# Kernel tuning notes

Measured on AMD Instinct MI355X. Metric: run time of the kernel, lower is better.

Reference implementation:

```python
import jax, jax.numpy as jnp
from jax import lax
import numpy as np

H = 256

def _cell(x, h, c, wih, whh, bih, bhh):
    # PyTorch LSTMCell: gates ordered i, f, g, o
    g = x @ wih.T + bih + h @ whh.T + bhh
    i, f, gg, o = jnp.split(g, 4, axis=-1)
    c = jax.nn.sigmoid(f) * c + jax.nn.sigmoid(i) * jnp.tanh(gg)
    h = jax.nn.sigmoid(o) * jnp.tanh(c)
    return h, c


def setup_inputs() -> dict:
    key = jax.random.key(0)
    ks = iter(jax.random.split(key, 64))
    def lin(out_f, in_f):
        s = 1.0 / np.sqrt(in_f)
        w = jax.random.uniform(next(ks), (out_f, in_f), minval=-s, maxval=s, dtype=jnp.float32)
        b = jax.random.uniform(next(ks), (out_f,), minval=-s, maxval=s, dtype=jnp.float32)
        return w, b
    def cellp():
        s = 1.0 / np.sqrt(H)
        return tuple(jax.random.uniform(next(ks), sh, minval=-s, maxval=s, dtype=jnp.float32)
                     for sh in [(4 * H, H), (4 * H, H), (4 * H,), (4 * H,)])
    d = {}
    d['x'] = jax.random.normal(next(ks), (20, 256, 64, 64), dtype=jnp.float32)
    d['fc_en1_w'], d['fc_en1_b'] = lin(1024, 4096)
    d['fc_en2_w'], d['fc_en2_b'] = lin(H, 1024)
    for nm in ['en1', 'en2', 'en3', 'de1', 'de2', 'de3']:
        d[nm + '_wih'], d[nm + '_whh'], d[nm + '_bih'], d[nm + '_bhh'] = cellp()
    d['fc_de1_w'], d['fc_de1_b'] = lin(1024, H)
    d['fc_de2_w'], d['fc_de2_b'] = lin(4096, 1024)
    d['future_step'] = 10
    return d


def reference(x, fc_en1_w, fc_en1_b, fc_en2_w, fc_en2_b,
              en1_wih, en1_whh, en1_bih, en1_bhh,
              en2_wih, en2_whh, en2_bih, en2_bhh,
              en3_wih, en3_whh, en3_bih, en3_bhh,
              de1_wih, de1_whh, de1_bih, de1_bhh,
              de2_wih, de2_whh, de2_bih, de2_bhh,
              de3_wih, de3_whh, de3_bih, de3_bhh,
              fc_de1_w, fc_de1_b, fc_de2_w, fc_de2_b, future_step):
    seq, B = x.shape[0], x.shape[1]
    xf = x.reshape(seq, B, -1)  # (S, B, 4096)
    z0 = jnp.zeros((B, H), x.dtype)

    def enc_step(carry, xt):
        h1, c1, h2, c2, h3, c3 = carry
        z = jax.nn.relu(xt @ fc_en1_w.T + fc_en1_b)
        z = jax.nn.relu(z @ fc_en2_w.T + fc_en2_b)
        h1, c1 = _cell(z, h1, c1, en1_wih, en1_whh, en1_bih, en1_bhh)
        h2, c2 = _cell(h1, h2, c2, en2_wih, en2_whh, en2_bih, en2_bhh)
        h3, c3 = _cell(h2, h3, c3, en3_wih, en3_whh, en3_bih, en3_bhh)
        return (h1, c1, h2, c2, h3, c3), None

    enc_carry, _ = lax.scan(enc_step, (z0,) * 6, xf)
    h_e3 = enc_carry[4]

    def dec_step(carry, _):
        h1, c1, h2, c2, h3, c3 = carry
        h1, c1 = _cell(z0, h1, c1, de1_wih, de1_whh, de1_bih, de1_bhh)
        h2, c2 = _cell(h1, h2, c2, de2_wih, de2_whh, de2_bih, de2_bhh)
        h3, c3 = _cell(h2, h3, c3, de3_wih, de3_whh, de3_bih, de3_bhh)
        y = jax.nn.relu(h3 @ fc_de1_w.T + fc_de1_b)
        y = jnp.tanh(y @ fc_de2_w.T + fc_de2_b)
        return (h1, c1, h2, c2, h3, c3), y

    _, ys = lax.scan(dec_step, (h_e3, z0, z0, z0, z0, z0), None, length=future_step)
    return ys.reshape(future_step, B, 64, 64)
```

## Files before the change

### kernel.cpp

```cpp
#include <hip/hip_runtime.h>
#include <math.h>

static __device__ __forceinline__ float sigf(float v) { return 1.0f / (1.0f + expf(-v)); }

using s8v = __attribute__((ext_vector_type(8))) short;
using f4v = __attribute__((ext_vector_type(4))) float;

static __device__ __forceinline__ void splitf(float f, unsigned short& h, unsigned short& l) {
  unsigned u = __float_as_uint(f);
  unsigned short hb = (unsigned short)((u + 0x7FFFu + ((u >> 16) & 1u)) >> 16);
  float hf = __uint_as_float(((unsigned)hb) << 16);
  float lf = f - hf;
  unsigned ul = __float_as_uint(lf);
  unsigned short lb = (unsigned short)((ul + 0x7FFFu + ((ul >> 16) & 1u)) >> 16);
  h = hb; l = lb;
}

__global__ __launch_bounds__(256) void wsplit(
    const float* __restrict__ W, unsigned short* __restrict__ WH,
    unsigned short* __restrict__ WL, int n4)
{
  int i = blockIdx.x * 256 + threadIdx.x;
  if (i < n4) {
    float4 v = ((const float4*)W)[i];
    ushort4 h, l;
    splitf(v.x, h.x, l.x); splitf(v.y, h.y, l.y);
    splitf(v.z, h.z, l.z); splitf(v.w, h.w, l.w);
    ((ushort4*)WH)[i] = h;
    ((ushort4*)WL)[i] = l;
  }
}

template <int OSPLIT>
__global__ __launch_bounds__(256) void gemm_sf(
    const float* __restrict__ A,
    const unsigned short* __restrict__ WH, const unsigned short* __restrict__ WL,
    const float* __restrict__ bias, float* __restrict__ C,
    unsigned short* __restrict__ OH, unsigned short* __restrict__ OL,
    int M, int N, int K, int act)
{
  __shared__ unsigned short AsH[128 * 40];
  __shared__ unsigned short AsL[128 * 40];
  __shared__ unsigned short WsH[64 * 40];
  __shared__ unsigned short WsL[64 * 40];

  const int t = threadIdx.x;
  const int w = t >> 6, lane = t & 63;
  const int lrow = lane & 15, lk = (lane >> 4) * 8;
  const int m0 = blockIdx.x * 128, n0 = blockIdx.y * 64;

  f4v acc[2][4];
#pragma unroll
  for (int i = 0; i < 2; ++i)
#pragma unroll
    for (int j = 0; j < 4; ++j) acc[i][j] = (f4v){0.f, 0.f, 0.f, 0.f};

  for (int k0 = 0; k0 < K; k0 += 32) {
#pragma unroll
    for (int i = 0; i < 4; ++i) {
      int v = i * 256 + t;
      int row = v >> 3, kq = (v & 7) << 2;
      float4 a = *(const float4*)(A + (size_t)(m0 + row) * K + k0 + kq);
      ushort4 h4, l4;
      splitf(a.x, h4.x, l4.x); splitf(a.y, h4.y, l4.y);
      splitf(a.z, h4.z, l4.z); splitf(a.w, h4.w, l4.w);
      *(ushort4*)&AsH[row * 40 + kq] = h4;
      *(ushort4*)&AsL[row * 40 + kq] = l4;
    }
    {
      int row = t >> 2, q = (t & 3) * 8;
      *(s8v*)&WsH[row * 40 + q] = *(const s8v*)(WH + (size_t)(n0 + row) * K + k0 + q);
      *(s8v*)&WsL[row * 40 + q] = *(const s8v*)(WL + (size_t)(n0 + row) * K + k0 + q);
    }
    __syncthreads();

    s8v aH[2], aL[2], bH[4], bL[4];
#pragma unroll
    for (int mt = 0; mt < 2; ++mt) {
      int r = (w * 32 + mt * 16 + lrow) * 40 + lk;
      aH[mt] = *(const s8v*)&AsH[r];
      aL[mt] = *(const s8v*)&AsL[r];
    }
#pragma unroll
    for (int nt = 0; nt < 4; ++nt) {
      int r = (nt * 16 + lrow) * 40 + lk;
      bH[nt] = *(const s8v*)&WsH[r];
      bL[nt] = *(const s8v*)&WsL[r];
    }
#pragma unroll
    for (int mt = 0; mt < 2; ++mt)
#pragma unroll
      for (int nt = 0; nt < 4; ++nt) {
        acc[mt][nt] = __builtin_amdgcn_mfma_f32_16x16x32_bf16(aH[mt], bH[nt], acc[mt][nt], 0, 0, 0);
        acc[mt][nt] = __builtin_amdgcn_mfma_f32_16x16x32_bf16(aH[mt], bL[nt], acc[mt][nt], 0, 0, 0);
        acc[mt][nt] = __builtin_amdgcn_mfma_f32_16x16x32_bf16(aL[mt], bH[nt], acc[mt][nt], 0, 0, 0);
      }
    __syncthreads();
  }

#pragma unroll
  for (int mt = 0; mt < 2; ++mt)
#pragma unroll
    for (int nt = 0; nt < 4; ++nt) {
      int gcol = n0 + nt * 16 + lrow;
      float bv = bias[gcol];
#pragma unroll
      for (int r = 0; r < 4; ++r) {
        int grow = m0 + w * 32 + mt * 16 + (lane >> 4) * 4 + r;
        float v = acc[mt][nt][r] + bv;
        if (act == 1) v = fmaxf(v, 0.f);
        else if (act == 2) v = tanhf(v);
        if (OSPLIT) {
          unsigned short h, l;
          splitf(v, h, l);
          OH[(size_t)grow * N + gcol] = h;
          OL[(size_t)grow * N + gcol] = l;
        } else {
          C[(size_t)grow * N + gcol] = v;
        }
      }
    }
}

template <int OSPLIT>
__global__ __launch_bounds__(256) void gemm_bb(
    const unsigned short* __restrict__ AH, const unsigned short* __restrict__ AL,
    const unsigned short* __restrict__ WH, const unsigned short* __restrict__ WL,
    const float* __restrict__ bias, float* __restrict__ C,
    unsigned short* __restrict__ OH, unsigned short* __restrict__ OL,
    int M, int N, int K, int act)
{
  __shared__ unsigned short AsH[128 * 40];
  __shared__ unsigned short AsL[128 * 40];
  __shared__ unsigned short WsH[64 * 40];
  __shared__ unsigned short WsL[64 * 40];

  const int t = threadIdx.x;
  const int w = t >> 6, lane = t & 63;
  const int lrow = lane & 15, lk = (lane >> 4) * 8;
  const int m0 = blockIdx.x * 128, n0 = blockIdx.y * 64;

  f4v acc[2][4];
#pragma unroll
  for (int i = 0; i < 2; ++i)
#pragma unroll
    for (int j = 0; j < 4; ++j) acc[i][j] = (f4v){0.f, 0.f, 0.f, 0.f};

  for (int k0 = 0; k0 < K; k0 += 32) {
#pragma unroll
    for (int i = 0; i < 2; ++i) {
      int v = i * 256 + t;
      int row = v >> 2, q = (v & 3) * 8;
      *(s8v*)&AsH[row * 40 + q] = *(const s8v*)(AH + (size_t)(m0 + row) * K + k0 + q);
      *(s8v*)&AsL[row * 40 + q] = *(const s8v*)(AL + (size_t)(m0 + row) * K + k0 + q);
    }
    {
      int row = t >> 2, q = (t & 3) * 8;
      *(s8v*)&WsH[row * 40 + q] = *(const s8v*)(WH + (size_t)(n0 + row) * K + k0 + q);
      *(s8v*)&WsL[row * 40 + q] = *(const s8v*)(WL + (size_t)(n0 + row) * K + k0 + q);
    }
    __syncthreads();

    s8v aH[2], aL[2], bH[4], bL[4];
#pragma unroll
    for (int mt = 0; mt < 2; ++mt) {
      int r = (w * 32 + mt * 16 + lrow) * 40 + lk;
      aH[mt] = *(const s8v*)&AsH[r];
      aL[mt] = *(const s8v*)&AsL[r];
    }
#pragma unroll
    for (int nt = 0; nt < 4; ++nt) {
      int r = (nt * 16 + lrow) * 40 + lk;
      bH[nt] = *(const s8v*)&WsH[r];
      bL[nt] = *(const s8v*)&WsL[r];
    }
#pragma unroll
    for (int mt = 0; mt < 2; ++mt)
#pragma unroll
      for (int nt = 0; nt < 4; ++nt) {
        acc[mt][nt] = __builtin_amdgcn_mfma_f32_16x16x32_bf16(aH[mt], bH[nt], acc[mt][nt], 0, 0, 0);
        acc[mt][nt] = __builtin_amdgcn_mfma_f32_16x16x32_bf16(aH[mt], bL[nt], acc[mt][nt], 0, 0, 0);
        acc[mt][nt] = __builtin_amdgcn_mfma_f32_16x16x32_bf16(aL[mt], bH[nt], acc[mt][nt], 0, 0, 0);
      }
    __syncthreads();
  }

#pragma unroll
  for (int mt = 0; mt < 2; ++mt)
#pragma unroll
    for (int nt = 0; nt < 4; ++nt) {
      int gcol = n0 + nt * 16 + lrow;
      float bv = bias[gcol];
#pragma unroll
      for (int r = 0; r < 4; ++r) {
        int grow = m0 + w * 32 + mt * 16 + (lane >> 4) * 4 + r;
        float v = acc[mt][nt][r] + bv;
        if (act == 1) v = fmaxf(v, 0.f);
        else if (act == 2) v = tanhf(v);
        if (OSPLIT) {
          unsigned short h, l;
          splitf(v, h, l);
          OH[(size_t)grow * N + gcol] = h;
          OL[(size_t)grow * N + gcol] = l;
        } else {
          C[(size_t)grow * N + gcol] = v;
        }
      }
    }
}

__global__ __launch_bounds__(256) void prep_pack(
    const float* __restrict__ wih, const float* __restrict__ whh,
    const float* __restrict__ bih, const float* __restrict__ bhh,
    float* __restrict__ wihP, float* __restrict__ whhP, float* __restrict__ bP)
{
  const int j = blockIdx.x, k = threadIdx.x;
  float4 a, c;
  a.x = wih[(0 * 256 + j) * 256 + k];
  a.y = wih[(1 * 256 + j) * 256 + k];
  a.z = wih[(2 * 256 + j) * 256 + k];
  a.w = wih[(3 * 256 + j) * 256 + k];
  *(float4*)&wihP[((size_t)j * 256 + k) * 4] = a;
  c.x = whh[(0 * 256 + j) * 256 + k];
  c.y = whh[(1 * 256 + j) * 256 + k];
  c.z = whh[(2 * 256 + j) * 256 + k];
  c.w = whh[(3 * 256 + j) * 256 + k];
  *(float4*)&whhP[((size_t)j * 256 + k) * 4] = c;
  if (k < 4) bP[j * 4 + k] = bih[k * 256 + j] + bhh[k * 256 + j];
}

__global__ __launch_bounds__(256) void transpose256(
    const float* __restrict__ in, float* __restrict__ out)
{
  const int t = blockIdx.x, c4 = blockIdx.y;
  const int r = threadIdx.x;
  float4 v = *(const float4*)(in + ((size_t)t * 256 + r) * 256 + c4 * 4);
  float* op = out + (size_t)t * 65536 + (size_t)(c4 * 4) * 256 + r;
  op[0]   = v.x;
  op[256] = v.y;
  op[512] = v.z;
  op[768] = v.w;
}

__global__ __launch_bounds__(256) void transpose256s(
    const float* __restrict__ in, unsigned short* __restrict__ outH,
    unsigned short* __restrict__ outL)
{
  const int t = blockIdx.x, c4 = blockIdx.y;
  const int r = threadIdx.x;
  float4 v = *(const float4*)(in + ((size_t)t * 256 + r) * 256 + c4 * 4);
  ushort4 h, l;
  splitf(v.x, h.x, l.x); splitf(v.y, h.y, l.y);
  splitf(v.z, h.z, l.z); splitf(v.w, h.w, l.w);
  size_t o = (size_t)t * 65536 + (size_t)(c4 * 4) * 256 + r;
  outH[o] = h.x; outH[o + 256] = h.y; outH[o + 512] = h.z; outH[o + 768] = h.w;
  outL[o] = l.x; outL[o + 256] = l.y; outL[o + 512] = l.z; outL[o + 768] = l.w;
}

struct CellSlot {
  const float* x;
  const float* wih;
  const float* whh;
  const float* bias;
  const float* hin;
  float* c;
  float* hout;
  float* hcopy;
  int hasx;
};
struct CellArgs { CellSlot s[3]; };

__global__ __launch_bounds__(256) void cell_multi(CellArgs args)
{
  const CellSlot S = args.s[blockIdx.x >> 8];
  const int inner = blockIdx.x & 255;
  const int jg = inner & 63, bg = inner >> 6;
  const int t = threadIdx.x;
  const int lane = t & 63;
  const int b = bg * 64 + lane;

  const int jw = __builtin_amdgcn_readfirstlane(jg * 4 + (t >> 6));
  const float4* wh = (const float4*)(S.whh + (size_t)jw * 1024);
  const float4* wi = (const float4*)(S.wih + (size_t)jw * 1024);
  const float* hcol = S.hin + b;
  float4 acc = *(const float4*)(S.bias + jw * 4);

  if (S.hasx) {
    const float* xcol = S.x + b;
#pragma unroll 8
    for (int k = 0; k < 256; ++k) {
      const float hv = hcol[k * 256];
      const float4 wv = wh[k];
      acc.x = fmaf(hv, wv.x, acc.x);
      acc.y = fmaf(hv, wv.y, acc.y);
      acc.z = fmaf(hv, wv.z, acc.z);
      acc.w = fmaf(hv, wv.w, acc.w);
      const float xv = xcol[k * 256];
      const float4 vv = wi[k];
      acc.x = fmaf(xv, vv.x, acc.x);
      acc.y = fmaf(xv, vv.y, acc.y);
      acc.z = fmaf(xv, vv.z, acc.z);
      acc.w = fmaf(xv, vv.w, acc.w);
    }
  } else {
#pragma unroll 8
    for (int k = 0; k < 256; ++k) {
      const float hv = hcol[k * 256];
      const float4 wv = wh[k];
      acc.x = fmaf(hv, wv.x, acc.x);
      acc.y = fmaf(hv, wv.y, acc.y);
      acc.z = fmaf(hv, wv.z, acc.z);
      acc.w = fmaf(hv, wv.w, acc.w);
    }
  }

  const int idx = jw * 256 + b;
  const float cold = S.c[idx];
  const float ig = sigf(acc.x), fg = sigf(acc.y);
  const float gg = tanhf(acc.z), og = sigf(acc.w);
  const float cn = fg * cold + ig * gg;
  const float hn = og * tanhf(cn);
  S.c[idx] = cn;
  S.hout[idx] = hn;
  if (S.hcopy) S.hcopy[idx] = hn;
}


extern "C" void kernel_launch(void* const* d_in, const int* in_sizes, int n_in,
                              void* d_out, int out_size, void* d_ws, size_t ws_size,
                              hipStream_t stream)
{
  const float* x_in  = (const float*)d_in[0];
  const float* w_en1 = (const float*)d_in[1];
  const float* b_en1 = (const float*)d_in[2];
  const float* w_en2 = (const float*)d_in[3];
  const float* b_en2 = (const float*)d_in[4];
  const float* cw[6][4];
  for (int i = 0; i < 6; ++i)
    for (int j = 0; j < 4; ++j) cw[i][j] = (const float*)d_in[5 + i * 4 + j];
  const float* w_de1 = (const float*)d_in[29];
  const float* b_de1 = (const float*)d_in[30];
  const float* w_de2 = (const float*)d_in[31];
  const float* b_de2 = (const float*)d_in[32];
  float* out = (float*)d_out;

  float* ws   = (float*)d_ws;
  float* wihP = ws;
  float* whhP = wihP + 6 * 262144;
  float* bP   = whhP + 6 * 262144;
  float* hb   = bP + 6 * 1024;
  float* cb   = hb + 12 * 65536;
  float* H3T  = cb + 6 * 65536;
  float* z2   = H3T + 10 * 65536;
  float* z2T  = z2 + 1310720;
  unsigned short* us = (unsigned short*)(z2T + 1310720);
  unsigned short* WEN1H = us;              us += 4194304;
  unsigned short* WEN1L = us;              us += 4194304;
  unsigned short* WEN2H = us;              us += 262144;
  unsigned short* WEN2L = us;              us += 262144;
  unsigned short* WDE1H = us;              us += 262144;
  unsigned short* WDE1L = us;              us += 262144;
  unsigned short* WDE2H = us;              us += 4194304;
  unsigned short* WDE2L = us;              us += 4194304;
  unsigned short* Z1H   = us;              us += 5242880;
  unsigned short* Z1L   = us;              us += 5242880;
  unsigned short* H3H = Z1H;
  unsigned short* H3L = Z1H + 655360;
  unsigned short* Y1H = Z1H + 1310720;
  unsigned short* Y1L = Z1H + 1310720 + 2621440;

  for (int i = 0; i < 6; ++i)
    prep_pack<<<256, 256, 0, stream>>>(cw[i][0], cw[i][1], cw[i][2], cw[i][3],
                                       wihP + i * 262144, whhP + i * 262144,
                                       bP + i * 1024);
  wsplit<<<4096, 256, 0, stream>>>(w_en1, WEN1H, WEN1L, 1048576);
  wsplit<<<256, 256, 0, stream>>>(w_en2, WEN2H, WEN2L, 65536);
  wsplit<<<256, 256, 0, stream>>>(w_de1, WDE1H, WDE1L, 65536);
  wsplit<<<4096, 256, 0, stream>>>(w_de2, WDE2H, WDE2L, 1048576);
  hipMemsetAsync(hb, 0, (size_t)18 * 65536 * sizeof(float), stream);

  gemm_sf<1><<<dim3(5120 / 128, 1024 / 64), 256, 0, stream>>>(
      x_in, WEN1H, WEN1L, b_en1, nullptr, Z1H, Z1L, 5120, 1024, 4096, 1);
  gemm_bb<0><<<dim3(5120 / 128, 256 / 64), 256, 0, stream>>>(
      Z1H, Z1L, WEN2H, WEN2L, b_en2, z2, nullptr, nullptr, 5120, 256, 1024, 1);
  transpose256<<<dim3(20, 64), 256, 0, stream>>>(z2, z2T);

  int pp[6] = {0, 0, 0, 0, 0, 0};
  auto HBuf = [&](int l, int p) { return hb + (size_t)(l * 2 + p) * 65536; };
  auto CBuf = [&](int l) { return cb + (size_t)l * 65536; };
  auto WI = [&](int l) { return wihP + (size_t)l * 262144; };
  auto WH = [&](int l) { return whhP + (size_t)l * 262144; };
  auto BB = [&](int l) { return bP + (size_t)l * 1024; };

  for (int s = 0; s <= 21; ++s) {
    CellArgs a; int n = 0; int tog[3]; int nt = 0;
    if (s < 20) {
      a.s[n++] = {z2T + (size_t)s * 65536, WI(0), WH(0), BB(0),
                  HBuf(0, pp[0]), CBuf(0), HBuf(0, pp[0] ^ 1), nullptr, 1};
      tog[nt++] = 0;
    }
    if (s >= 1 && s <= 20) {
      a.s[n++] = {HBuf(0, pp[0]), WI(1), WH(1), BB(1),
                  HBuf(1, pp[1]), CBuf(1), HBuf(1, pp[1] ^ 1), nullptr, 1};
      tog[nt++] = 1;
    }
    if (s >= 2) {
      a.s[n++] = {HBuf(1, pp[1]), WI(2), WH(2), BB(2),
                  HBuf(2, pp[2]), CBuf(2), HBuf(2, pp[2] ^ 1), nullptr, 1};
      tog[nt++] = 2;
    }
    cell_multi<<<n * 256, 256, 0, stream>>>(a);
    for (int i = 0; i < nt; ++i) pp[tog[i]] ^= 1;
  }

  for (int s = 0; s <= 11; ++s) {
    CellArgs a; int n = 0; int tog[3]; int nt = 0;
    if (s < 10) {
      const float* h1in = (s == 0) ? HBuf(2, pp[2]) : HBuf(3, pp[3]);
      a.s[n++] = {nullptr, WI(3), WH(3), BB(3),
                  h1in, CBuf(3), HBuf(3, pp[3] ^ 1), nullptr, 0};
      tog[nt++] = 3;
    }
    if (s >= 1 && s <= 10) {
      a.s[n++] = {HBuf(3, pp[3]), WI(4), WH(4), BB(4),
                  HBuf(4, pp[4]), CBuf(4), HBuf(4, pp[4] ^ 1), nullptr, 1};
      tog[nt++] = 4;
    }
    if (s >= 2) {
      a.s[n++] = {HBuf(4, pp[4]), WI(5), WH(5), BB(5),
                  HBuf(5, pp[5]), CBuf(5), HBuf(5, pp[5] ^ 1),
                  H3T + (size_t)(s - 2) * 65536, 1};
      tog[nt++] = 5;
    }
    cell_multi<<<n * 256, 256, 0, stream>>>(a);
    for (int i = 0; i < nt; ++i) pp[tog[i]] ^= 1;
  }

  transpose256s<<<dim3(10, 64), 256, 0, stream>>>(H3T, H3H, H3L);
  gemm_bb<1><<<dim3(2560 / 128, 1024 / 64), 256, 0, stream>>>(
      H3H, H3L, WDE1H, WDE1L, b_de1, nullptr, Y1H, Y1L, 2560, 1024, 256, 1);
  gemm_bb<0><<<dim3(2560 / 128, 4096 / 64), 256, 0, stream>>>(
      Y1H, Y1L, WDE2H, WDE2L, b_de2, out, nullptr, nullptr, 2560, 4096, 1024, 2);

  (void)in_sizes; (void)n_in; (void)out_size; (void)ws_size;
}
```

Baseline: 945.5 us.

## Hoist encoder layer-1 input projection into a batched GEMM and pre-split input

The layer-1 encoder input projection (z @ W_ih^T + bias) for all 20 timesteps is now computed up front by one MFMA GEMM that writes gate-packed preactivations, so each recurrent step only does the h @ W_hh part for that layer. The z2 transpose kernel is removed, and the second encoder GEMM now emits bf16 hi/lo split output directly. When workspace allows, x is also pre-split into bf16 hi/lo so the first GEMM uses the bf16-input kernel. This adds a large extra pass over x and more workspace in exchange for shorter sequential cell steps.

```diff
diff --git a/kernel.cpp b/kernel.cpp
--- a/kernel.cpp
+++ b/kernel.cpp
@@ -122,12 +122,13 @@
     }
 }
 
-template <int OSPLIT>
+template <int OMODE>
 __global__ __launch_bounds__(256) void gemm_bb(
     const unsigned short* __restrict__ AH, const unsigned short* __restrict__ AL,
     const unsigned short* __restrict__ WH, const unsigned short* __restrict__ WL,
     const float* __restrict__ bias, float* __restrict__ C,
     unsigned short* __restrict__ OH, unsigned short* __restrict__ OL,
+    float* __restrict__ XG,
     int M, int N, int K, int act)
 {
   __shared__ unsigned short AsH[128 * 40];
@@ -190,20 +191,26 @@
 #pragma unroll
     for (int nt = 0; nt < 4; ++nt) {
       int gcol = n0 + nt * 16 + lrow;
-      float bv = bias[gcol];
 #pragma unroll
       for (int r = 0; r < 4; ++r) {
         int grow = m0 + w * 32 + mt * 16 + (lane >> 4) * 4 + r;
-        float v = acc[mt][nt][r] + bv;
-        if (act == 1) v = fmaxf(v, 0.f);
-        else if (act == 2) v = tanhf(v);
-        if (OSPLIT) {
-          unsigned short h, l;
-          splitf(v, h, l);
-          OH[(size_t)grow * N + gcol] = h;
-          OL[(size_t)grow * N + gcol] = l;
+        if (OMODE == 2) {
+          int tt = grow >> 8, bb = grow & 255;
+          int ss = gcol >> 8, jj = gcol & 255;
+          float v = acc[mt][nt][r] + bias[jj * 4 + ss];
+          XG[(((size_t)tt * 256 + jj) * 256 + bb) * 4 + ss] = v;
         } else {
-          C[(size_t)grow * N + gcol] = v;
+          float v = acc[mt][nt][r] + bias[gcol];
+          if (act == 1) v = fmaxf(v, 0.f);
+          else if (act == 2) v = tanhf(v);
+          if (OMODE == 1) {
+            unsigned short h, l;
+            splitf(v, h, l);
+            OH[(size_t)grow * N + gcol] = h;
+            OL[(size_t)grow * N + gcol] = l;
+          } else {
+            C[(size_t)grow * N + gcol] = v;
+          }
         }
       }
     }
@@ -229,19 +236,6 @@
   if (k < 4) bP[j * 4 + k] = bih[k * 256 + j] + bhh[k * 256 + j];
 }
 
-__global__ __launch_bounds__(256) void transpose256(
-    const float* __restrict__ in, float* __restrict__ out)
-{
-  const int t = blockIdx.x, c4 = blockIdx.y;
-  const int r = threadIdx.x;
-  float4 v = *(const float4*)(in + ((size_t)t * 256 + r) * 256 + c4 * 4);
-  float* op = out + (size_t)t * 65536 + (size_t)(c4 * 4) * 256 + r;
-  op[0]   = v.x;
-  op[256] = v.y;
-  op[512] = v.z;
-  op[768] = v.w;
-}
-
 __global__ __launch_bounds__(256) void transpose256s(
     const float* __restrict__ in, unsigned short* __restrict__ outH,
     unsigned short* __restrict__ outL)
@@ -258,6 +252,7 @@
 }
 
 struct CellSlot {
+  const float* xg;
   const float* x;
   const float* wih;
   const float* whh;
@@ -283,7 +278,9 @@
   const float4* wh = (const float4*)(S.whh + (size_t)jw * 1024);
   const float4* wi = (const float4*)(S.wih + (size_t)jw * 1024);
   const float* hcol = S.hin + b;
-  float4 acc = *(const float4*)(S.bias + jw * 4);
+  float4 acc;
+  if (S.xg) acc = ((const float4*)S.xg)[jw * 256 + b];
+  else      acc = *(const float4*)(S.bias + jw * 4);
 
   if (S.hasx) {
     const float* xcol = S.x + b;
@@ -344,16 +341,15 @@
   const float* b_de2 = (const float*)d_in[32];
   float* out = (float*)d_out;
 
-  float* ws   = (float*)d_ws;
-  float* wihP = ws;
+  float* fs   = (float*)d_ws;
+  float* wihP = fs;
   float* whhP = wihP + 6 * 262144;
   float* bP   = whhP + 6 * 262144;
   float* hb   = bP + 6 * 1024;
   float* cb   = hb + 12 * 65536;
   float* H3T  = cb + 6 * 65536;
-  float* z2   = H3T + 10 * 65536;
-  float* z2T  = z2 + 1310720;
-  unsigned short* us = (unsigned short*)(z2T + 1310720);
+  float* R    = H3T + 10 * 65536;
+  unsigned short* us = (unsigned short*)(R + 5242880);
   unsigned short* WEN1H = us;              us += 4194304;
   unsigned short* WEN1L = us;              us += 4194304;
   unsigned short* WEN2H = us;              us += 262144;
@@ -362,12 +358,22 @@
   unsigned short* WDE1L = us;              us += 262144;
   unsigned short* WDE2H = us;              us += 4194304;
   unsigned short* WDE2L = us;              us += 4194304;
-  unsigned short* Z1H   = us;              us += 5242880;
-  unsigned short* Z1L   = us;              us += 5242880;
-  unsigned short* H3H = Z1H;
-  unsigned short* H3L = Z1H + 655360;
-  unsigned short* Y1H = Z1H + 1310720;
-  unsigned short* Y1L = Z1H + 1310720 + 2621440;
+  unsigned short* WIH0H = us;              us += 262144;
+  unsigned short* WIH0L = us;              us += 262144;
+  unsigned short* Z2H   = us;              us += 1310720;
+  unsigned short* Z2L   = us;              us += 1310720;
+  unsigned short* XH    = us;              us += 20971520;
+  unsigned short* XL    = us;              us += 20971520;
+  const size_t need_big = (size_t)((char*)us - (char*)d_ws);
+  const bool big = ws_size >= need_big;
+
+  unsigned short* Z1H = (unsigned short*)R;
+  unsigned short* Z1L = Z1H + 5242880;
+  float* XG = R;
+  unsigned short* H3H = (unsigned short*)R;
+  unsigned short* H3L = H3H + 655360;
+  unsigned short* Y1H = H3H + 1310720;
+  unsigned short* Y1L = Y1H + 2621440;
 
   for (int i = 0; i < 6; ++i)
     prep_pack<<<256, 256, 0, stream>>>(cw[i][0], cw[i][1], cw[i][2], cw[i][3],
@@ -377,35 +383,43 @@
   wsplit<<<256, 256, 0, stream>>>(w_en2, WEN2H, WEN2L, 65536);
   wsplit<<<256, 256, 0, stream>>>(w_de1, WDE1H, WDE1L, 65536);
   wsplit<<<4096, 256, 0, stream>>>(w_de2, WDE2H, WDE2L, 1048576);
+  wsplit<<<256, 256, 0, stream>>>(cw[0][0], WIH0H, WIH0L, 65536);
+  if (big)
+    wsplit<<<20480, 256, 0, stream>>>(x_in, XH, XL, 5242880);
   hipMemsetAsync(hb, 0, (size_t)18 * 65536 * sizeof(float), stream);
 
-  gemm_sf<1><<<dim3(5120 / 128, 1024 / 64), 256, 0, stream>>>(
-      x_in, WEN1H, WEN1L, b_en1, nullptr, Z1H, Z1L, 5120, 1024, 4096, 1);
-  gemm_bb<0><<<dim3(5120 / 128, 256 / 64), 256, 0, stream>>>(
-      Z1H, Z1L, WEN2H, WEN2L, b_en2, z2, nullptr, nullptr, 5120, 256, 1024, 1);
-  transpose256<<<dim3(20, 64), 256, 0, stream>>>(z2, z2T);
+  if (big)
+    gemm_bb<1><<<dim3(40, 16), 256, 0, stream>>>(
+        XH, XL, WEN1H, WEN1L, b_en1, nullptr, Z1H, Z1L, nullptr, 5120, 1024, 4096, 1);
+  else
+    gemm_sf<1><<<dim3(40, 16), 256, 0, stream>>>(
+        x_in, WEN1H, WEN1L, b_en1, nullptr, Z1H, Z1L, 5120, 1024, 4096, 1);
+  gemm_bb<1><<<dim3(40, 4), 256, 0, stream>>>(
+      Z1H, Z1L, WEN2H, WEN2L, b_en2, nullptr, Z2H, Z2L, nullptr, 5120, 256, 1024, 1);
+  gemm_bb<2><<<dim3(40, 16), 256, 0, stream>>>(
+      Z2H, Z2L, WIH0H, WIH0L, bP, nullptr, nullptr, nullptr, XG, 5120, 1024, 256, 0);
 
   int pp[6] = {0, 0, 0, 0, 0, 0};
   auto HBuf = [&](int l, int p) { return hb + (size_t)(l * 2 + p) * 65536; };
   auto CBuf = [&](int l) { return cb + (size_t)l * 65536; };
   auto WI = [&](int l) { return wihP + (size_t)l * 262144; };
-  auto WH = [&](int l) { return whhP + (size_t)l * 262144; };
+  auto WHp = [&](int l) { return whhP + (size_t)l * 262144; };
   auto BB = [&](int l) { return bP + (size_t)l * 1024; };
 
   for (int s = 0; s <= 21; ++s) {
     CellArgs a; int n = 0; int tog[3]; int nt = 0;
     if (s < 20) {
-      a.s[n++] = {z2T + (size_t)s * 65536, WI(0), WH(0), BB(0),
-                  HBuf(0, pp[0]), CBuf(0), HBuf(0, pp[0] ^ 1), nullptr, 1};
+      a.s[n++] = {XG + (size_t)s * 262144, nullptr, WI(0), WHp(0), BB(0),
+                  HBuf(0, pp[0]), CBuf(0), HBuf(0, pp[0] ^ 1), nullptr, 0};
       tog[nt++] = 0;
     }
     if (s >= 1 && s <= 20) {
-      a.s[n++] = {HBuf(0, pp[0]), WI(1), WH(1), BB(1),
+      a.s[n++] = {nullptr, HBuf(0, pp[0]), WI(1), WHp(1), BB(1),
                   HBuf(1, pp[1]), CBuf(1), HBuf(1, pp[1] ^ 1), nullptr, 1};
       tog[nt++] = 1;
     }
     if (s >= 2) {
-      a.s[n++] = {HBuf(1, pp[1]), WI(2), WH(2), BB(2),
+      a.s[n++] = {nullptr, HBuf(1, pp[1]), WI(2), WHp(2), BB(2),
                   HBuf(2, pp[2]), CBuf(2), HBuf(2, pp[2] ^ 1), nullptr, 1};
       tog[nt++] = 2;
     }
@@ -417,17 +431,17 @@
     CellArgs a; int n = 0; int tog[3]; int nt = 0;
     if (s < 10) {
       const float* h1in = (s == 0) ? HBuf(2, pp[2]) : HBuf(3, pp[3]);
-      a.s[n++] = {nullptr, WI(3), WH(3), BB(3),
+      a.s[n++] = {nullptr, nullptr, WI(3), WHp(3), BB(3),
                   h1in, CBuf(3), HBuf(3, pp[3] ^ 1), nullptr, 0};
       tog[nt++] = 3;
     }
     if (s >= 1 && s <= 10) {
-      a.s[n++] = {HBuf(3, pp[3]), WI(4), WH(4), BB(4),
+      a.s[n++] = {nullptr, HBuf(3, pp[3]), WI(4), WHp(4), BB(4),
                   HBuf(4, pp[4]), CBuf(4), HBuf(4, pp[4] ^ 1), nullptr, 1};
       tog[nt++] = 4;
     }
     if (s >= 2) {
-      a.s[n++] = {HBuf(4, pp[4]), WI(5), WH(5), BB(5),
+      a.s[n++] = {nullptr, HBuf(4, pp[4]), WI(5), WHp(5), BB(5),
                   HBuf(5, pp[5]), CBuf(5), HBuf(5, pp[5] ^ 1),
                   H3T + (size_t)(s - 2) * 65536, 1};
       tog[nt++] = 5;
@@ -437,10 +451,10 @@
   }
 
   transpose256s<<<dim3(10, 64), 256, 0, stream>>>(H3T, H3H, H3L);
-  gemm_bb<1><<<dim3(2560 / 128, 1024 / 64), 256, 0, stream>>>(
-      H3H, H3L, WDE1H, WDE1L, b_de1, nullptr, Y1H, Y1L, 2560, 1024, 256, 1);
-  gemm_bb<0><<<dim3(2560 / 128, 4096 / 64), 256, 0, stream>>>(
-      Y1H, Y1L, WDE2H, WDE2L, b_de2, out, nullptr, nullptr, 2560, 4096, 1024, 2);
+  gemm_bb<1><<<dim3(20, 16), 256, 0, stream>>>(
+      H3H, H3L, WDE1H, WDE1L, b_de1, nullptr, Y1H, Y1L, nullptr, 2560, 1024, 256, 1);
+  gemm_bb<0><<<dim3(20, 64), 256, 0, stream>>>(
+      Y1H, Y1L, WDE2H, WDE2L, b_de2, out, nullptr, nullptr, nullptr, 2560, 4096, 1024, 2);
 
   (void)in_sizes; (void)n_in; (void)out_size; (void)ws_size;
 }
```

Result: slower. 1.089 ms (+15.2%).
